# Kernel tuning notes

Hardware: AMD Instinct MI355X
Metric: run time of the kernel (lower is better)

The kernel has to match this reference:

```python
import jax, jax.numpy as jnp
import numpy as np

D = 64
NU = 30000
NI = 20000
LU = 50  # mailbox length at user nodes (item_max_length)
LI = 50  # mailbox length at item nodes (user_max_length)


def setup_inputs() -> dict:
    key = jax.random.key(0)
    ks = jax.random.split(key, 14)
    s = 0.05
    return {
        "user_feat": jax.random.normal(ks[0], (NU, D), jnp.float32),
        "item_feat": jax.random.normal(ks[1], (NI, D), jnp.float32),
        "W_u": jax.random.normal(ks[2], (D, D), jnp.float32) * s,
        "W_i": jax.random.normal(ks[3], (D, D), jnp.float32) * s,
        "Wg_u": jax.random.normal(ks[4], (2 * D, D), jnp.float32) * s,
        "Wg_i": jax.random.normal(ks[5], (2 * D, D), jnp.float32) * s,
        "i_te": jax.random.normal(ks[6], (LI, D), jnp.float32) * s,
        "i_te_k": jax.random.normal(ks[7], (LI, D), jnp.float32) * s,
        "u_te": jax.random.normal(ks[8], (LU, D), jnp.float32) * s,
        "u_te_k": jax.random.normal(ks[9], (LU, D), jnp.float32) * s,
        "item_nbr": jax.random.randint(ks[10], (NI, LI), 0, NU, jnp.int32),
        "item_time": jax.random.randint(ks[11], (NI, LI), 0, 1000000, jnp.int32),
        "user_nbr": jax.random.randint(ks[12], (NU, LU), 0, NI, jnp.int32),
        "user_time": jax.random.randint(ks[13], (NU, LU), 0, 1000000, jnp.int32),
    }


def _orgat_att(src_mb, dst_h, time, te, te_k):
    """One DGSR reduce: long-term time-encoded attention + short-term last-attention.
    src_mb: [N, L, d] gathered source features; dst_h: [N, d]; time: [N, L] int.
    Returns concat([h_long, h_short]) @ Wg applied by caller.
    """
    L = time.shape[1]
    d = src_mb.shape[-1]
    scale = jnp.sqrt(jnp.asarray(d, src_mb.dtype))
    # rank of each edge's time within the neighborhood; re_order: 0 = most recent
    rank = jnp.argsort(jnp.argsort(time, axis=1), axis=1)
    re_o = L - rank - 1                                       # [N, L]
    e = jnp.sum((te[re_o] + src_mb) * dst_h[:, None, :], axis=2) / scale
    alpha = jax.nn.softmax(e, axis=1)                         # [N, L]
    h_long = jnp.sum(alpha[..., None] * (src_mb + te_k[re_o]), axis=1)
    # short-term: attention keyed on the most-recent neighbor
    last = jnp.argmax(time, axis=1)
    last_em = jnp.take_along_axis(src_mb, last[:, None, None], axis=1)  # [N,1,d]
    e1 = jnp.sum(last_em * src_mb, axis=2) / scale
    a1 = jax.nn.softmax(e1, axis=1)
    h_short = jnp.sum(a1[..., None] * src_mb, axis=1)
    return jnp.concatenate([h_long, h_short], axis=-1)        # [N, 2d]


def reference(user_feat, item_feat, W_u, W_i, Wg_u, Wg_i, i_te, i_te_k,
              u_te, u_te_k, item_nbr, item_time, user_nbr, user_time):
    uh = user_feat @ W_u   # user_weight (feat_drop=0)
    ih = item_feat @ W_i   # item_weight
    # 'by' edges: users -> items (item reduce uses user mailboxes + i_time_encoding)
    u_mb = uh[item_nbr]                                        # [NI, LI, d]
    item_new = _orgat_att(u_mb, ih, item_time, i_te, i_te_k) @ Wg_i
    # 'pby' edges: items -> users (user reduce uses item mailboxes + u_time_encoding)
    i_mb = ih[user_nbr]                                        # [NU, LU, d]
    user_new = _orgat_att(i_mb, uh, user_time, u_te, u_te_k) @ Wg_u
    # residual update functions
    user_out = jax.nn.elu(user_new + user_feat)
    item_out = jax.nn.elu(item_new + item_feat)
    return user_out, item_out
```

## Files before the change

### kernel.cpp

```cpp
#include <hip/hip_runtime.h>
#include <stdint.h>

#define D   64
#define L   50
#define NUM_U 30000
#define NUM_I 20000


typedef __attribute__((ext_vector_type(8))) short short8x;
typedef __attribute__((ext_vector_type(4))) float f32x4;

__device__ __forceinline__ float lof(unsigned int u) {
    union { unsigned int i; float f; } v; v.i = u << 16; return v.f;
}
__device__ __forceinline__ float hif(unsigned int u) {
    union { unsigned int i; float f; } v; v.i = u & 0xffff0000u; return v.f;
}
__device__ __forceinline__ unsigned int f2bfbits(float f) {
    union { float f; unsigned int i; } v; v.f = f;
    return (v.i + 0x7fffu + ((v.i >> 16) & 1u)) >> 16;
}
__device__ __forceinline__ unsigned int packbf(float a, float b) {
    return f2bfbits(a) | (f2bfbits(b) << 16);
}
__device__ __forceinline__ float rl(float v, int l) {
    return __int_as_float(__builtin_amdgcn_readlane(__float_as_int(v), l));
}
__device__ __forceinline__ int rli(int v, int l) {
    return __builtin_amdgcn_readlane(v, l);
}

__global__ void pack_aux(const float* __restrict__ Wg_i, const float* __restrict__ Wg_u,
                         const float* __restrict__ te_i, const float* __restrict__ te_u,
                         const float* __restrict__ tk_i, const float* __restrict__ tk_u,
                         unsigned short* __restrict__ WgPi, unsigned short* __restrict__ WgPu,
                         unsigned short* __restrict__ tePi, unsigned short* __restrict__ tePu,
                         unsigned short* __restrict__ tkPi, unsigned short* __restrict__ tkPu)
{
    int gid = blockIdx.x * 256 + threadIdx.x, gs = gridDim.x * 256;
    for (int idx = gid; idx < 8192; idx += gs) {
        int n = idx >> 7, k = idx & 127;
        WgPi[idx] = (unsigned short)f2bfbits(Wg_i[k * 64 + n]);
        WgPu[idx] = (unsigned short)f2bfbits(Wg_u[k * 64 + n]);
    }
    for (int idx = gid; idx < 4096; idx += gs) {
        int r = idx >> 6, k = idx & 63;
        tePi[idx] = (r < L) ? (unsigned short)f2bfbits(te_i[r * 64 + k]) : 0;
        tePu[idx] = (r < L) ? (unsigned short)f2bfbits(te_u[r * 64 + k]) : 0;
        int d = idx >> 6, rr = idx & 63;
        tkPi[idx] = (rr < L) ? (unsigned short)f2bfbits(tk_i[rr * 64 + d]) : 0;
        tkPu[idx] = (rr < L) ? (unsigned short)f2bfbits(tk_u[rr * 64 + d]) : 0;
    }
}

__global__ __launch_bounds__(256) void gemm_h(
    const float* __restrict__ user_feat,
    const float* __restrict__ item_feat,
    const float* __restrict__ W_u,
    const float* __restrict__ W_i,
    unsigned int* __restrict__ H)
{
    const int tid = threadIdx.x, lane = tid & 63, wid = tid >> 6;
    int r0 = blockIdx.x * 16 + wid * 4;
    const float* src; const float* W;
    if (r0 < NUM_U) { src = user_feat + (size_t)r0 * D;            W = W_u; }
    else            { src = item_feat + (size_t)(r0 - NUM_U) * D;  W = W_i; }

    float f0 = src[0 * D + lane], f1 = src[1 * D + lane];
    float f2 = src[2 * D + lane], f3 = src[3 * D + lane];
    float a0 = 0.f, a1 = 0.f, a2 = 0.f, a3 = 0.f;
#pragma unroll
    for (int k = 0; k < 64; k++) {
        float wk = W[k * 64 + lane];
        a0 += rl(f0, k) * wk; a1 += rl(f1, k) * wk;
        a2 += rl(f2, k) * wk; a3 += rl(f3, k) * wk;
    }
    int li = (lane & 31) << 1;
    float p0 = __shfl(a0, li), q0 = __shfl(a0, li | 1);
    float p1 = __shfl(a1, li), q1 = __shfl(a1, li | 1);
    float p2 = __shfl(a2, li), q2 = __shfl(a2, li | 1);
    float p3 = __shfl(a3, li), q3 = __shfl(a3, li | 1);
    if (lane < 32) {
        H[(size_t)(r0 + 0) * 32 + lane] = packbf(p0, q0);
        H[(size_t)(r0 + 1) * 32 + lane] = packbf(p1, q1);
        H[(size_t)(r0 + 2) * 32 + lane] = packbf(p2, q2);
        H[(size_t)(r0 + 3) * 32 + lane] = packbf(p3, q3);
    }
}

__global__ __launch_bounds__(256, 4) void attn_ws(
    const unsigned int* __restrict__ H,
    int src_base, int dst_base,
    const float* __restrict__ dst_feat,
    const unsigned short* __restrict__ WgP,
    const unsigned short* __restrict__ teP,
    const unsigned short* __restrict__ tekP,
    const int* __restrict__ nbr,
    const int* __restrict__ timev,
    float* __restrict__ out)
{
    __shared__ unsigned int   mbs[4][56 * 33];
    __shared__ float          esc[4][192];
    __shared__ unsigned short ala[4][192];
    __shared__ unsigned short dhlm[4][128];
    __shared__ unsigned short cat16[4][136];

    const int tid = threadIdx.x, lane = tid & 63, wid = tid >> 6;
    const int n = blockIdx.x * 4 + wid;
    const int q4 = lane >> 4, c16 = lane & 15;

    unsigned int* mbw = mbs[wid];
    unsigned short* mbw_sh = (unsigned short*)mbw;

    for (int p = lane; p < 198; p += 64) mbw[1650 + p] = 0;

    int t   = (lane < L) ? timev[(size_t)n * L + lane] : 0;
    int nbv = (lane < L) ? nbr[(size_t)n * L + lane]  : 0;
    unsigned int key  = (lane < L) ? ((((unsigned)t) << 6) | (unsigned)lane) : 0u;
    unsigned int key2 = (lane < L) ? ((((unsigned)t) << 6) | (unsigned)(63 - lane)) : 0u;

    int rank = 0;
#pragma unroll
    for (int j = 0; j < L; j++) {
        unsigned int kj = (unsigned int)rli((int)key, j);
        rank += (kj < key) ? 1 : 0;
    }
    int re_o = (lane < L) ? (L - 1 - rank) : lane;

    unsigned int m2 = key2;
#pragma unroll
    for (int s = 32; s; s >>= 1) { unsigned int o2 = __shfl_xor(m2, s); m2 = (o2 > m2) ? o2 : m2; }
    const int last = 63 - (int)(m2 & 63u);

    unsigned int ud = H[(size_t)(dst_base + n) * 32 + (lane >> 1)];
    float dh = (lane & 1) ? hif(ud) : lof(ud);
    dhlm[wid][lane] = (unsigned short)f2bfbits(dh);

    {
        const unsigned int* Hs = H + (size_t)src_base * 32;
        int half = lane >> 5, col = lane & 31;
#pragma unroll
        for (int l = 0; l < L; l += 2) {
            int ra = rli(nbv, l), rb = rli(nbv, l + 1);
            int r = half ? rb : ra;
            mbw[(l + half) * 33 + col] = Hs[(size_t)r * 32 + col];
        }
    }

    unsigned int ulm = mbw[last * 33 + (lane >> 1)];
    float lm = (lane & 1) ? hif(ulm) : lof(ulm);
    dhlm[wid][64 + lane] = (unsigned short)f2bfbits(lm);

    f32x4 zero4 = {0.f, 0.f, 0.f, 0.f};
    f32x4 acc_e[4], acc_t[4];
#pragma unroll
    for (int nt = 0; nt < 4; nt++) { acc_e[nt] = zero4; acc_t[nt] = zero4; }
    {
        const unsigned short* dl = dhlm[wid];
#pragma unroll
        for (int kt = 0; kt < 2; kt++) {
            short8x afr = *(const short8x*)(dl + (c16 & 1) * 64 + kt * 32 + q4 * 8);
#pragma unroll
            for (int nt = 0; nt < 4; nt++) {
                int row = c16 + 16 * nt;
                union { short8x v; unsigned int u[4]; } bu;
                int base = row * 33 + kt * 16 + q4 * 4;
                bu.u[0] = mbw[base + 0]; bu.u[1] = mbw[base + 1];
                bu.u[2] = mbw[base + 2]; bu.u[3] = mbw[base + 3];
                acc_e[nt] = __builtin_amdgcn_mfma_f32_16x16x32_bf16(afr, bu.v, acc_e[nt], 0, 0, 0);
                short8x bt = *(const short8x*)(teP + row * 64 + kt * 32 + q4 * 8);
                acc_t[nt] = __builtin_amdgcn_mfma_f32_16x16x32_bf16(afr, bt, acc_t[nt], 0, 0, 0);
            }
        }
    }
    if (q4 == 0) {
#pragma unroll
        for (int nt = 0; nt < 4; nt++) {
            esc[wid][c16 + 16 * nt]       = acc_e[nt][0];
            esc[wid][64 + c16 + 16 * nt]  = acc_e[nt][1];
            esc[wid][128 + c16 + 16 * nt] = acc_t[nt][0];
        }
    }
    float e  = esc[wid][lane];
    float e1 = esc[wid][64 + lane];
    float th = esc[wid][128 + re_o];

    e = (e + th) * 0.125f;
    e1 *= 0.125f;
    if (lane >= L) { e = -3e38f; e1 = -3e38f; }

    float mx = e;
#pragma unroll
    for (int s = 32; s; s >>= 1) { float o2 = __shfl_xor(mx, s); mx = (o2 > mx) ? o2 : mx; }
    float ex = __expf(e - mx);
    float sm = ex;
#pragma unroll
    for (int s = 32; s; s >>= 1) sm += __shfl_xor(sm, s);
    float alpha = ex / sm;

    float mx1 = e1;
#pragma unroll
    for (int s = 32; s; s >>= 1) { float o2 = __shfl_xor(mx1, s); mx1 = (o2 > mx1) ? o2 : mx1; }
    float ex1 = __expf(e1 - mx1);
    float sm1 = ex1;
#pragma unroll
    for (int s = 32; s; s >>= 1) sm1 += __shfl_xor(sm1, s);
    float aw = ex1 / sm1;

    ala[wid][lane]        = (unsigned short)f2bfbits(alpha);
    ala[wid][64 + lane]   = (unsigned short)f2bfbits(aw);
    ala[wid][128 + re_o]  = (unsigned short)f2bfbits(alpha);

    f32x4 acc_s[4], acc_k[4];
#pragma unroll
    for (int nt = 0; nt < 4; nt++) { acc_s[nt] = zero4; acc_k[nt] = zero4; }
    {
        const unsigned short* alp = ala[wid];
#pragma unroll
        for (int kt = 0; kt < 2; kt++) {
            short8x aS = *(const short8x*)(alp + (c16 & 1) * 64 + kt * 32 + q4 * 8);
            short8x aB = *(const short8x*)(alp + 128 + kt * 32 + q4 * 8);
#pragma unroll
            for (int nt = 0; nt < 4; nt++) {
                int dcol = c16 + 16 * nt;
                short8x bM;
                if (kt == 0) {
                    int b0 = (q4 * 8) * 66 + dcol;
#pragma unroll
                    for (int i = 0; i < 8; i++) bM[i] = (short)mbw_sh[b0 + i * 66];
                } else {
#pragma unroll
                    for (int i = 0; i < 8; i++) {
                        int k = 32 + q4 * 8 + i;
                        int kk = (k < L) ? k : L;
                        bM[i] = (short)mbw_sh[kk * 66 + dcol];
                    }
                }
                acc_s[nt] = __builtin_amdgcn_mfma_f32_16x16x32_bf16(aS, bM, acc_s[nt], 0, 0, 0);
                short8x bK = *(const short8x*)(tekP + dcol * 64 + kt * 32 + q4 * 8);
                acc_k[nt] = __builtin_amdgcn_mfma_f32_16x16x32_bf16(aB, bK, acc_k[nt], 0, 0, 0);
            }
        }
    }
    if (q4 == 0) {
#pragma unroll
        for (int nt = 0; nt < 4; nt++) {
            cat16[wid][c16 + 16 * nt]      = (unsigned short)f2bfbits(acc_s[nt][0] + acc_k[nt][0]);
            cat16[wid][64 + c16 + 16 * nt] = (unsigned short)f2bfbits(acc_s[nt][1]);
        }
    }
    __syncthreads();

    short8x bfr[4];
#pragma unroll
    for (int tK = 0; tK < 4; tK++)
        bfr[tK] = *(const short8x*)(WgP + (wid * 16 + c16) * 128 + tK * 32 + q4 * 8);

    f32x4 acc = zero4;
#pragma unroll
    for (int tK = 0; tK < 4; tK++) {
        short8x a = *(const short8x*)(&cat16[lane & 3][tK * 32 + q4 * 8]);
        acc = __builtin_amdgcn_mfma_f32_16x16x32_bf16(a, bfr[tK], acc, 0, 0, 0);
    }
    float r01 = (q4 & 1) ? acc[1] : acc[0];
    float r23 = (q4 & 1) ? acc[3] : acc[2];
    float pv  = (q4 & 2) ? r23 : r01;

    int node = blockIdx.x * 4 + q4;
    float fres = dst_feat[(size_t)node * D + wid * 16 + c16];
    float oo = pv + fres;
    oo = (oo > 0.f) ? oo : (__expf(oo) - 1.f);
    out[(size_t)node * D + wid * 16 + c16] = oo;
}

__global__ __launch_bounds__(256) void attn_mono(
    const float* __restrict__ src_feat, const float* __restrict__ dst_feat,
    const float* __restrict__ W_src, const float* __restrict__ W_dst,
    const float* __restrict__ Wg, const float* __restrict__ te,
    const float* __restrict__ tek, const int* __restrict__ nbr,
    const int* __restrict__ timev, float* __restrict__ out)
{
    __shared__ unsigned int ws32[64 * 33];
    __shared__ unsigned int te32[L * 33];
    __shared__ unsigned int mbs[4][L * 33];
    const int tid = threadIdx.x, lane = tid & 63, wid = tid >> 6;
    const int n = blockIdx.x * 4 + wid;
    {
        const float2* Wf2 = (const float2*)W_src;
        const float2* Te2 = (const float2*)te;
        for (int idx = tid; idx < 2048; idx += 256) {
            float2 w = Wf2[idx];
            ws32[(idx >> 5) * 33 + (idx & 31)] = packbf(w.x, w.y);
            if (idx < 1600) {
                float2 t2 = Te2[idx];
                te32[(idx >> 5) * 33 + (idx & 31)] = packbf(t2.x, t2.y);
            }
        }
    }
    __syncthreads();
    int t  = (lane < L) ? timev[(size_t)n * L + lane] : 0;
    int nb = (lane < L) ? nbr[(size_t)n * L + lane]  : 0;
    unsigned int key  = (lane < L) ? ((((unsigned)t) << 6) | (unsigned)lane) : 0u;
    unsigned int key2 = (lane < L) ? ((((unsigned)t) << 6) | (unsigned)(63 - lane)) : 0u;
    int rank = 0;
#pragma unroll
    for (int j = 0; j < L; j++) {
        unsigned int kj = (unsigned int)rli((int)key, j);
        rank += (kj < key) ? 1 : 0;
    }
    int re_o = (lane < L) ? (L - 1 - rank) : 0;
    unsigned int m2 = key2;
#pragma unroll
    for (int s = 32; s; s >>= 1) { unsigned int o2 = __shfl_xor(m2, s); m2 = (o2 > m2) ? o2 : m2; }
    const int last = 63 - (int)(m2 & 63u);
    const int rr = (lane < L) ? lane : (L - 1);
    float f = dst_feat[(size_t)n * D + lane];
    float dh;
    {
        float b0 = 0.f, b1 = 0.f, b2 = 0.f, b3 = 0.f;
#pragma unroll
        for (int k = 0; k < 64; k += 4) {
            b0 += rl(f, k + 0) * W_dst[(k + 0) * 64 + lane];
            b1 += rl(f, k + 1) * W_dst[(k + 1) * 64 + lane];
            b2 += rl(f, k + 2) * W_dst[(k + 2) * 64 + lane];
            b3 += rl(f, k + 3) * W_dst[(k + 3) * 64 + lane];
        }
        dh = (b0 + b1) + (b2 + b3);
    }
    float v1;
    {
        float b0 = 0.f, b1 = 0.f, b2 = 0.f, b3 = 0.f;
#pragma unroll
        for (int j = 0; j < 32; j += 2) {
            unsigned int u0 = ws32[lane * 33 + j];
            unsigned int u1 = ws32[lane * 33 + j + 1];
            b0 += lof(u0) * rl(dh, 2 * j + 0);
            b1 += hif(u0) * rl(dh, 2 * j + 1);
            b2 += lof(u1) * rl(dh, 2 * j + 2);
            b3 += hif(u1) * rl(dh, 2 * j + 3);
        }
        v1 = (b0 + b1) + (b2 + b3);
    }
    unsigned int* mbw = mbs[wid];
    {
        const float2* src2 = (const float2*)src_feat;
        int half = lane >> 5, col = lane & 31;
#pragma unroll
        for (int l = 0; l < L; l += 2) {
            int ra = rli(nb, l), rb = rli(nb, l + 1);
            int r = half ? rb : ra;
            float2 v = src2[(size_t)r * 32 + col];
            mbw[(l + half) * 33 + col] = packbf(v.x, v.y);
        }
    }
    __syncthreads();
    unsigned int ul = mbw[last * 33 + (lane >> 1)];
    float rlast = (lane & 1) ? hif(ul) : lof(ul);
    float g;
    {
        float b0 = 0.f, b1 = 0.f, b2 = 0.f, b3 = 0.f;
#pragma unroll
        for (int k = 0; k < 64; k += 4) {
            b0 += rl(rlast, k + 0) * W_src[(k + 0) * 64 + lane];
            b1 += rl(rlast, k + 1) * W_src[(k + 1) * 64 + lane];
            b2 += rl(rlast, k + 2) * W_src[(k + 2) * 64 + lane];
            b3 += rl(rlast, k + 3) * W_src[(k + 3) * 64 + lane];
        }
        g = (b0 + b1) + (b2 + b3);
    }
    float v2;
    {
        float b0 = 0.f, b1 = 0.f, b2 = 0.f, b3 = 0.f;
#pragma unroll
        for (int j = 0; j < 32; j += 2) {
            unsigned int u0 = ws32[lane * 33 + j];
            unsigned int u1 = ws32[lane * 33 + j + 1];
            b0 += lof(u0) * rl(g, 2 * j + 0);
            b1 += hif(u0) * rl(g, 2 * j + 1);
            b2 += lof(u1) * rl(g, 2 * j + 2);
            b3 += hif(u1) * rl(g, 2 * j + 3);
        }
        v2 = (b0 + b1) + (b2 + b3);
    }
    float teh;
    {
        float b0 = 0.f, b1 = 0.f, b2 = 0.f, b3 = 0.f;
#pragma unroll
        for (int j = 0; j < 32; j += 2) {
            unsigned int u0 = te32[rr * 33 + j];
            unsigned int u1 = te32[rr * 33 + j + 1];
            b0 += lof(u0) * rl(dh, 2 * j + 0);
            b1 += hif(u0) * rl(dh, 2 * j + 1);
            b2 += lof(u1) * rl(dh, 2 * j + 2);
            b3 += hif(u1) * rl(dh, 2 * j + 3);
        }
        teh = (b0 + b1) + (b2 + b3);
    }
    float e, e1;
    {
        float ea = 0.f, eb = 0.f, qa = 0.f, qb = 0.f;
#pragma unroll
        for (int j = 0; j < 32; j += 2) {
            unsigned int u0 = mbw[rr * 33 + j];
            unsigned int u1 = mbw[rr * 33 + j + 1];
            float m0 = lof(u0), m1 = hif(u0), m2f = lof(u1), m3 = hif(u1);
            ea += m0 * rl(v1, 2 * j + 0) + m1 * rl(v1, 2 * j + 1);
            eb += m2f * rl(v1, 2 * j + 2) + m3 * rl(v1, 2 * j + 3);
            qa += m0 * rl(v2, 2 * j + 0) + m1 * rl(v2, 2 * j + 1);
            qb += m2f * rl(v2, 2 * j + 2) + m3 * rl(v2, 2 * j + 3);
        }
        e = ea + eb; e1 = qa + qb;
    }
    e = (e + __shfl(teh, re_o)) * 0.125f;
    e1 *= 0.125f;
    if (lane >= L) { e = -3e38f; e1 = -3e38f; }
    float mx = e;
#pragma unroll
    for (int s = 32; s; s >>= 1) { float o2 = __shfl_xor(mx, s); mx = (o2 > mx) ? o2 : mx; }
    float ex = __expf(e - mx);
    float sm = ex;
#pragma unroll
    for (int s = 32; s; s >>= 1) sm += __shfl_xor(sm, s);
    float alpha = ex / sm;
    float mx1 = e1;
#pragma unroll
    for (int s = 32; s; s >>= 1) { float o2 = __shfl_xor(mx1, s); mx1 = (o2 > mx1) ? o2 : mx1; }
    float ex1 = __expf(e1 - mx1);
    float sm1 = ex1;
#pragma unroll
    for (int s = 32; s; s >>= 1) sm1 += __shfl_xor(sm1, s);
    float aw = ex1 / sm1;
    float sl, ss, tacc;
    {
        float sA = 0.f, sB = 0.f, hA = 0.f, hB = 0.f, tA = 0.f, tB = 0.f;
        int hcol = lane >> 1, odd = lane & 1;
#pragma unroll
        for (int l = 0; l < L; l += 2) {
            float saA = rl(alpha, l),     s1A = rl(aw, l);
            float saB = rl(alpha, l + 1), s1B = rl(aw, l + 1);
            int   roA = rli(re_o, l),     roB = rli(re_o, l + 1);
            unsigned int uA = mbw[(l + 0) * 33 + hcol];
            unsigned int uB = mbw[(l + 1) * 33 + hcol];
            float mA = odd ? hif(uA) : lof(uA);
            float mB = odd ? hif(uB) : lof(uB);
            sA += saA * mA; hA += s1A * mA; tA += saA * tek[roA * 64 + lane];
            sB += saB * mB; hB += s1B * mB; tB += saB * tek[roB * 64 + lane];
        }
        sl = sA + sB; ss = hA + hB; tacc = tA + tB;
    }
    float hl, hs;
    {
        float lA = 0.f, lB = 0.f, sA = 0.f, sB = 0.f;
#pragma unroll
        for (int k = 0; k < 64; k += 2) {
            float w0 = W_src[(k + 0) * 64 + lane];
            float w1 = W_src[(k + 1) * 64 + lane];
            lA += rl(sl, k + 0) * w0; sA += rl(ss, k + 0) * w0;
            lB += rl(sl, k + 1) * w1; sB += rl(ss, k + 1) * w1;
        }
        hl = tacc + lA + lB; hs = sA + sB;
    }
    float o;
    {
        float o0 = 0.f, o1 = 0.f, o2 = 0.f, o3 = 0.f;
#pragma unroll
        for (int k = 0; k < 64; k += 2) {
            o0 += rl(hl, k + 0) * Wg[(k + 0) * 64 + lane];
            o1 += rl(hl, k + 1) * Wg[(k + 1) * 64 + lane];
            o2 += rl(hs, k + 0) * Wg[(k + 64) * 64 + lane];
            o3 += rl(hs, k + 1) * Wg[(k + 65) * 64 + lane];
        }
        o = f + (o0 + o1) + (o2 + o3);
    }
    o = (o > 0.f) ? o : (__expf(o) - 1.f);
    out[(size_t)n * D + lane] = o;
}

extern "C" void kernel_launch(void* const* d_in, const int* in_sizes, int n_in,
                              void* d_out, int out_size, void* d_ws, size_t ws_size,
                              hipStream_t stream) {
    const float* user_feat = (const float*)d_in[0];
    const float* item_feat = (const float*)d_in[1];
    const float* W_u  = (const float*)d_in[2];
    const float* W_i  = (const float*)d_in[3];
    const float* Wg_u = (const float*)d_in[4];
    const float* Wg_i = (const float*)d_in[5];
    const float* i_te   = (const float*)d_in[6];
    const float* i_te_k = (const float*)d_in[7];
    const float* u_te   = (const float*)d_in[8];
    const float* u_te_k = (const float*)d_in[9];
    const int* item_nbr  = (const int*)d_in[10];
    const int* item_time = (const int*)d_in[11];
    const int* user_nbr  = (const int*)d_in[12];
    const int* user_time = (const int*)d_in[13];
    (void)in_sizes; (void)n_in; (void)out_size;

    float* outp = (float*)d_out;
    const size_t H_BYTES = (size_t)(NUM_U + NUM_I) * 32 * 4;
    const size_t NEED = H_BYTES + 2 * 16384 + 4 * 8192;

    if (ws_size >= NEED) {
        unsigned int* Hp = (unsigned int*)d_ws;
        unsigned char* aux = (unsigned char*)d_ws + H_BYTES;
        unsigned short* WgPi = (unsigned short*)(aux);
        unsigned short* WgPu = (unsigned short*)(aux + 16384);
        unsigned short* tePi = (unsigned short*)(aux + 32768);
        unsigned short* tePu = (unsigned short*)(aux + 40960);
        unsigned short* tkPi = (unsigned short*)(aux + 49152);
        unsigned short* tkPu = (unsigned short*)(aux + 57344);

        pack_aux<<<16, 256, 0, stream>>>(Wg_i, Wg_u, i_te, u_te, i_te_k, u_te_k,
                                         WgPi, WgPu, tePi, tePu, tkPi, tkPu);
        gemm_h<<<(NUM_U + NUM_I) / 16, 256, 0, stream>>>(
            user_feat, item_feat, W_u, W_i, Hp);
        attn_ws<<<NUM_I / 4, 256, 0, stream>>>(
            Hp, 0, NUM_U, item_feat, WgPi, tePi, tkPi,
            item_nbr, item_time, outp + (size_t)NUM_U * D);
        attn_ws<<<NUM_U / 4, 256, 0, stream>>>(
            Hp, NUM_U, 0, user_feat, WgPu, tePu, tkPu,
            user_nbr, user_time, outp);
    } else {
        attn_mono<<<NUM_I / 4, 256, 0, stream>>>(
            user_feat, item_feat, W_u, W_i, Wg_i, i_te, i_te_k,
            item_nbr, item_time, outp + (size_t)NUM_U * D);
        attn_mono<<<NUM_U / 4, 256, 0, stream>>>(
            item_feat, user_feat, W_i, W_u, Wg_u, u_te, u_te_k,
            user_nbr, user_time, outp);
    }
}
```

Before: 245.0 us.

## Merge prep kernels and fuse item/user attention launches with compact LDS layout

```diff
diff --git a/kernel.cpp b/kernel.cpp
--- a/kernel.cpp
+++ b/kernel.cpp
@@ -5,6 +5,7 @@
 #define L   50
 #define NUM_U 30000
 #define NUM_I 20000
+#define PW  1976
 
 
 typedef __attribute__((ext_vector_type(8))) short short8x;
@@ -30,89 +31,99 @@
     return __builtin_amdgcn_readlane(v, l);
 }
 
-__global__ void pack_aux(const float* __restrict__ Wg_i, const float* __restrict__ Wg_u,
-                         const float* __restrict__ te_i, const float* __restrict__ te_u,
-                         const float* __restrict__ tk_i, const float* __restrict__ tk_u,
-                         unsigned short* __restrict__ WgPi, unsigned short* __restrict__ WgPu,
-                         unsigned short* __restrict__ tePi, unsigned short* __restrict__ tePu,
-                         unsigned short* __restrict__ tkPi, unsigned short* __restrict__ tkPu)
+__global__ __launch_bounds__(256) void prep(
+    const float* __restrict__ user_feat, const float* __restrict__ item_feat,
+    const float* __restrict__ W_u, const float* __restrict__ W_i,
+    const float* __restrict__ Wg_i, const float* __restrict__ Wg_u,
+    const float* __restrict__ te_i, const float* __restrict__ te_u,
+    const float* __restrict__ tk_i, const float* __restrict__ tk_u,
+    unsigned int* __restrict__ H,
+    unsigned short* __restrict__ WgPi, unsigned short* __restrict__ WgPu,
+    unsigned short* __restrict__ tePi, unsigned short* __restrict__ tePu,
+    unsigned short* __restrict__ tkPi, unsigned short* __restrict__ tkPu)
 {
-    int gid = blockIdx.x * 256 + threadIdx.x, gs = gridDim.x * 256;
-    for (int idx = gid; idx < 8192; idx += gs) {
-        int n = idx >> 7, k = idx & 127;
-        WgPi[idx] = (unsigned short)f2bfbits(Wg_i[k * 64 + n]);
-        WgPu[idx] = (unsigned short)f2bfbits(Wg_u[k * 64 + n]);
-    }
-    for (int idx = gid; idx < 4096; idx += gs) {
-        int r = idx >> 6, k = idx & 63;
-        tePi[idx] = (r < L) ? (unsigned short)f2bfbits(te_i[r * 64 + k]) : 0;
-        tePu[idx] = (r < L) ? (unsigned short)f2bfbits(te_u[r * 64 + k]) : 0;
-        int d = idx >> 6, rr = idx & 63;
-        tkPi[idx] = (rr < L) ? (unsigned short)f2bfbits(tk_i[rr * 64 + d]) : 0;
-        tkPu[idx] = (rr < L) ? (unsigned short)f2bfbits(tk_u[rr * 64 + d]) : 0;
-    }
-}
-
-__global__ __launch_bounds__(256) void gemm_h(
-    const float* __restrict__ user_feat,
-    const float* __restrict__ item_feat,
-    const float* __restrict__ W_u,
-    const float* __restrict__ W_i,
-    unsigned int* __restrict__ H)
-{
-    const int tid = threadIdx.x, lane = tid & 63, wid = tid >> 6;
-    int r0 = blockIdx.x * 16 + wid * 4;
-    const float* src; const float* W;
-    if (r0 < NUM_U) { src = user_feat + (size_t)r0 * D;            W = W_u; }
-    else            { src = item_feat + (size_t)(r0 - NUM_U) * D;  W = W_i; }
-
-    float f0 = src[0 * D + lane], f1 = src[1 * D + lane];
-    float f2 = src[2 * D + lane], f3 = src[3 * D + lane];
-    float a0 = 0.f, a1 = 0.f, a2 = 0.f, a3 = 0.f;
-#pragma unroll
-    for (int k = 0; k < 64; k++) {
-        float wk = W[k * 64 + lane];
-        a0 += rl(f0, k) * wk; a1 += rl(f1, k) * wk;
-        a2 += rl(f2, k) * wk; a3 += rl(f3, k) * wk;
-    }
-    int li = (lane & 31) << 1;
-    float p0 = __shfl(a0, li), q0 = __shfl(a0, li | 1);
-    float p1 = __shfl(a1, li), q1 = __shfl(a1, li | 1);
-    float p2 = __shfl(a2, li), q2 = __shfl(a2, li | 1);
-    float p3 = __shfl(a3, li), q3 = __shfl(a3, li | 1);
-    if (lane < 32) {
-        H[(size_t)(r0 + 0) * 32 + lane] = packbf(p0, q0);
-        H[(size_t)(r0 + 1) * 32 + lane] = packbf(p1, q1);
-        H[(size_t)(r0 + 2) * 32 + lane] = packbf(p2, q2);
-        H[(size_t)(r0 + 3) * 32 + lane] = packbf(p3, q3);
-    }
-}
-
-__global__ __launch_bounds__(256, 4) void attn_ws(
+    const int tid = threadIdx.x;
+    if (blockIdx.x < 3125) {
+        const int lane = tid & 63, wid = tid >> 6;
+        int r0 = blockIdx.x * 16 + wid * 4;
+        const float* src; const float* W;
+        if (r0 < NUM_U) { src = user_feat + (size_t)r0 * D;            W = W_u; }
+        else            { src = item_feat + (size_t)(r0 - NUM_U) * D;  W = W_i; }
+        float f0 = src[0 * D + lane], f1 = src[1 * D + lane];
+        float f2 = src[2 * D + lane], f3 = src[3 * D + lane];
+        float a0 = 0.f, a1 = 0.f, a2 = 0.f, a3 = 0.f;
+#pragma unroll
+        for (int k = 0; k < 64; k++) {
+            float wk = W[k * 64 + lane];
+            a0 += rl(f0, k) * wk; a1 += rl(f1, k) * wk;
+            a2 += rl(f2, k) * wk; a3 += rl(f3, k) * wk;
+        }
+        int li = (lane & 31) << 1;
+        float p0 = __shfl(a0, li), q0 = __shfl(a0, li | 1);
+        float p1 = __shfl(a1, li), q1 = __shfl(a1, li | 1);
+        float p2 = __shfl(a2, li), q2 = __shfl(a2, li | 1);
+        float p3 = __shfl(a3, li), q3 = __shfl(a3, li | 1);
+        if (lane < 32) {
+            H[(size_t)(r0 + 0) * 32 + lane] = packbf(p0, q0);
+            H[(size_t)(r0 + 1) * 32 + lane] = packbf(p1, q1);
+            H[(size_t)(r0 + 2) * 32 + lane] = packbf(p2, q2);
+            H[(size_t)(r0 + 3) * 32 + lane] = packbf(p3, q3);
+        }
+    } else {
+        int gid = (blockIdx.x - 3125) * 256 + tid;
+        for (int idx = gid; idx < 8192; idx += 4096) {
+            int n = idx >> 7, k = idx & 127;
+            WgPi[idx] = (unsigned short)f2bfbits(Wg_i[k * 64 + n]);
+            WgPu[idx] = (unsigned short)f2bfbits(Wg_u[k * 64 + n]);
+        }
+        {
+            int idx = gid;
+            int r = idx >> 6, k = idx & 63;
+            tePi[idx] = (r < L) ? (unsigned short)f2bfbits(te_i[r * 64 + k]) : 0;
+            tePu[idx] = (r < L) ? (unsigned short)f2bfbits(te_u[r * 64 + k]) : 0;
+            int d = idx >> 6, rr = idx & 63;
+            tkPi[idx] = (rr < L) ? (unsigned short)f2bfbits(tk_i[rr * 64 + d]) : 0;
+            tkPu[idx] = (rr < L) ? (unsigned short)f2bfbits(tk_u[rr * 64 + d]) : 0;
+        }
+    }
+}
+
+__global__ __launch_bounds__(256, 5) void attn_fused(
     const unsigned int* __restrict__ H,
-    int src_base, int dst_base,
-    const float* __restrict__ dst_feat,
-    const unsigned short* __restrict__ WgP,
-    const unsigned short* __restrict__ teP,
-    const unsigned short* __restrict__ tekP,
-    const int* __restrict__ nbr,
-    const int* __restrict__ timev,
+    const float* __restrict__ user_feat, const float* __restrict__ item_feat,
+    const unsigned short* __restrict__ WgPi, const unsigned short* __restrict__ WgPu,
+    const unsigned short* __restrict__ tePi, const unsigned short* __restrict__ tePu,
+    const unsigned short* __restrict__ tkPi, const unsigned short* __restrict__ tkPu,
+    const int* __restrict__ item_nbr, const int* __restrict__ item_time,
+    const int* __restrict__ user_nbr, const int* __restrict__ user_time,
     float* __restrict__ out)
 {
-    __shared__ unsigned int   mbs[4][56 * 33];
-    __shared__ float          esc[4][192];
-    __shared__ unsigned short ala[4][192];
-    __shared__ unsigned short dhlm[4][128];
-    __shared__ unsigned short cat16[4][136];
+    __shared__ unsigned int lds[4 * PW];
 
     const int tid = threadIdx.x, lane = tid & 63, wid = tid >> 6;
-    const int n = blockIdx.x * 4 + wid;
+    const bool iside = blockIdx.x < (NUM_I / 4);
+    const int bb = iside ? blockIdx.x : blockIdx.x - NUM_I / 4;
+    const int n = bb * 4 + wid;
+    const int src_base = iside ? 0 : NUM_U;
+    const int dst_base = iside ? NUM_U : 0;
+    const float* dst_feat = iside ? item_feat : user_feat;
+    const unsigned short* WgP  = iside ? WgPi : WgPu;
+    const unsigned short* teP  = iside ? tePi : tePu;
+    const unsigned short* tekP = iside ? tkPi : tkPu;
+    const int* nbr   = iside ? item_nbr  : user_nbr;
+    const int* timev = iside ? item_time : user_time;
+    float* outp = out + (iside ? (size_t)NUM_U * D : 0);
+
     const int q4 = lane >> 4, c16 = lane & 15;
 
-    unsigned int* mbw = mbs[wid];
+    unsigned int*   wld    = lds + wid * PW;
+    unsigned int*   mbw    = wld;
     unsigned short* mbw_sh = (unsigned short*)mbw;
-
-    for (int p = lane; p < 198; p += 64) mbw[1650 + p] = 0;
+    float*          escf   = (float*)(wld + 1684);
+    unsigned short* cat    = (unsigned short*)(wld + 1684);
+    unsigned short* dla    = (unsigned short*)(wld + 1876);
+
+    if (lane < 33) mbw[1650 + lane] = 0;
 
     int t   = (lane < L) ? timev[(size_t)n * L + lane] : 0;
     int nbv = (lane < L) ? nbr[(size_t)n * L + lane]  : 0;
@@ -134,7 +145,7 @@
 
     unsigned int ud = H[(size_t)(dst_base + n) * 32 + (lane >> 1)];
     float dh = (lane & 1) ? hif(ud) : lof(ud);
-    dhlm[wid][lane] = (unsigned short)f2bfbits(dh);
+    dla[lane] = (unsigned short)f2bfbits(dh);
 
     {
         const unsigned int* Hs = H + (size_t)src_base * 32;
@@ -149,41 +160,39 @@
 
     unsigned int ulm = mbw[last * 33 + (lane >> 1)];
     float lm = (lane & 1) ? hif(ulm) : lof(ulm);
-    dhlm[wid][64 + lane] = (unsigned short)f2bfbits(lm);
+    dla[64 + lane] = (unsigned short)f2bfbits(lm);
 
     f32x4 zero4 = {0.f, 0.f, 0.f, 0.f};
     f32x4 acc_e[4], acc_t[4];
 #pragma unroll
     for (int nt = 0; nt < 4; nt++) { acc_e[nt] = zero4; acc_t[nt] = zero4; }
-    {
-        const unsigned short* dl = dhlm[wid];
-#pragma unroll
-        for (int kt = 0; kt < 2; kt++) {
-            short8x afr = *(const short8x*)(dl + (c16 & 1) * 64 + kt * 32 + q4 * 8);
-#pragma unroll
-            for (int nt = 0; nt < 4; nt++) {
-                int row = c16 + 16 * nt;
-                union { short8x v; unsigned int u[4]; } bu;
-                int base = row * 33 + kt * 16 + q4 * 4;
-                bu.u[0] = mbw[base + 0]; bu.u[1] = mbw[base + 1];
-                bu.u[2] = mbw[base + 2]; bu.u[3] = mbw[base + 3];
-                acc_e[nt] = __builtin_amdgcn_mfma_f32_16x16x32_bf16(afr, bu.v, acc_e[nt], 0, 0, 0);
-                short8x bt = *(const short8x*)(teP + row * 64 + kt * 32 + q4 * 8);
-                acc_t[nt] = __builtin_amdgcn_mfma_f32_16x16x32_bf16(afr, bt, acc_t[nt], 0, 0, 0);
-            }
+#pragma unroll
+    for (int kt = 0; kt < 2; kt++) {
+        short8x afr = *(const short8x*)(dla + (c16 & 1) * 64 + kt * 32 + q4 * 8);
+#pragma unroll
+        for (int nt = 0; nt < 4; nt++) {
+            int row = c16 + 16 * nt;
+            int rowc = (row > 50) ? 50 : row;
+            union { short8x v; unsigned int u[4]; } bu;
+            int base = rowc * 33 + kt * 16 + q4 * 4;
+            bu.u[0] = mbw[base + 0]; bu.u[1] = mbw[base + 1];
+            bu.u[2] = mbw[base + 2]; bu.u[3] = mbw[base + 3];
+            acc_e[nt] = __builtin_amdgcn_mfma_f32_16x16x32_bf16(afr, bu.v, acc_e[nt], 0, 0, 0);
+            short8x bt = *(const short8x*)(teP + row * 64 + kt * 32 + q4 * 8);
+            acc_t[nt] = __builtin_amdgcn_mfma_f32_16x16x32_bf16(afr, bt, acc_t[nt], 0, 0, 0);
         }
     }
     if (q4 == 0) {
 #pragma unroll
         for (int nt = 0; nt < 4; nt++) {
-            esc[wid][c16 + 16 * nt]       = acc_e[nt][0];
-            esc[wid][64 + c16 + 16 * nt]  = acc_e[nt][1];
-            esc[wid][128 + c16 + 16 * nt] = acc_t[nt][0];
-        }
-    }
-    float e  = esc[wid][lane];
-    float e1 = esc[wid][64 + lane];
-    float th = esc[wid][128 + re_o];
+            escf[c16 + 16 * nt]       = acc_e[nt][0];
+            escf[64 + c16 + 16 * nt]  = acc_e[nt][1];
+            escf[128 + c16 + 16 * nt] = acc_t[nt][0];
+        }
+    }
+    float e  = escf[lane];
+    float e1 = escf[64 + lane];
+    float th = escf[128 + re_o];
 
     e = (e + th) * 0.125f;
     e1 *= 0.125f;
@@ -207,46 +216,43 @@
     for (int s = 32; s; s >>= 1) sm1 += __shfl_xor(sm1, s);
     float aw = ex1 / sm1;
 
-    ala[wid][lane]        = (unsigned short)f2bfbits(alpha);
-    ala[wid][64 + lane]   = (unsigned short)f2bfbits(aw);
-    ala[wid][128 + re_o]  = (unsigned short)f2bfbits(alpha);
+    dla[lane]       = (unsigned short)f2bfbits(alpha);
+    dla[64 + lane]  = (unsigned short)f2bfbits(aw);
+    dla[128 + re_o] = (unsigned short)f2bfbits(alpha);
 
     f32x4 acc_s[4], acc_k[4];
 #pragma unroll
     for (int nt = 0; nt < 4; nt++) { acc_s[nt] = zero4; acc_k[nt] = zero4; }
-    {
-        const unsigned short* alp = ala[wid];
-#pragma unroll
-        for (int kt = 0; kt < 2; kt++) {
-            short8x aS = *(const short8x*)(alp + (c16 & 1) * 64 + kt * 32 + q4 * 8);
-            short8x aB = *(const short8x*)(alp + 128 + kt * 32 + q4 * 8);
-#pragma unroll
-            for (int nt = 0; nt < 4; nt++) {
-                int dcol = c16 + 16 * nt;
-                short8x bM;
-                if (kt == 0) {
-                    int b0 = (q4 * 8) * 66 + dcol;
-#pragma unroll
-                    for (int i = 0; i < 8; i++) bM[i] = (short)mbw_sh[b0 + i * 66];
-                } else {
-#pragma unroll
-                    for (int i = 0; i < 8; i++) {
-                        int k = 32 + q4 * 8 + i;
-                        int kk = (k < L) ? k : L;
-                        bM[i] = (short)mbw_sh[kk * 66 + dcol];
-                    }
+#pragma unroll
+    for (int kt = 0; kt < 2; kt++) {
+        short8x aS = *(const short8x*)(dla + (c16 & 1) * 64 + kt * 32 + q4 * 8);
+        short8x aB = *(const short8x*)(dla + 128 + kt * 32 + q4 * 8);
+#pragma unroll
+        for (int nt = 0; nt < 4; nt++) {
+            int dcol = c16 + 16 * nt;
+            short8x bM;
+            if (kt == 0) {
+                int b0 = (q4 * 8) * 66 + dcol;
+#pragma unroll
+                for (int i = 0; i < 8; i++) bM[i] = (short)mbw_sh[b0 + i * 66];
+            } else {
+#pragma unroll
+                for (int i = 0; i < 8; i++) {
+                    int k = 32 + q4 * 8 + i;
+                    int kk = (k < L) ? k : 50;
+                    bM[i] = (short)mbw_sh[kk * 66 + dcol];
                 }
-                acc_s[nt] = __builtin_amdgcn_mfma_f32_16x16x32_bf16(aS, bM, acc_s[nt], 0, 0, 0);
-                short8x bK = *(const short8x*)(tekP + dcol * 64 + kt * 32 + q4 * 8);
-                acc_k[nt] = __builtin_amdgcn_mfma_f32_16x16x32_bf16(aB, bK, acc_k[nt], 0, 0, 0);
             }
+            acc_s[nt] = __builtin_amdgcn_mfma_f32_16x16x32_bf16(aS, bM, acc_s[nt], 0, 0, 0);
+            short8x bK = *(const short8x*)(tekP + dcol * 64 + kt * 32 + q4 * 8);
+            acc_k[nt] = __builtin_amdgcn_mfma_f32_16x16x32_bf16(aB, bK, acc_k[nt], 0, 0, 0);
         }
     }
     if (q4 == 0) {
 #pragma unroll
         for (int nt = 0; nt < 4; nt++) {
-            cat16[wid][c16 + 16 * nt]      = (unsigned short)f2bfbits(acc_s[nt][0] + acc_k[nt][0]);
-            cat16[wid][64 + c16 + 16 * nt] = (unsigned short)f2bfbits(acc_s[nt][1]);
+            cat[c16 + 16 * nt]      = (unsigned short)f2bfbits(acc_s[nt][0] + acc_k[nt][0]);
+            cat[64 + c16 + 16 * nt] = (unsigned short)f2bfbits(acc_s[nt][1]);
         }
     }
     __syncthreads();
@@ -256,21 +262,22 @@
     for (int tK = 0; tK < 4; tK++)
         bfr[tK] = *(const short8x*)(WgP + (wid * 16 + c16) * 128 + tK * 32 + q4 * 8);
 
+    const unsigned short* catw = (const unsigned short*)(lds + (lane & 3) * PW + 1684);
     f32x4 acc = zero4;
 #pragma unroll
     for (int tK = 0; tK < 4; tK++) {
-        short8x a = *(const short8x*)(&cat16[lane & 3][tK * 32 + q4 * 8]);
+        short8x a = *(const short8x*)(catw + tK * 32 + q4 * 8);
         acc = __builtin_amdgcn_mfma_f32_16x16x32_bf16(a, bfr[tK], acc, 0, 0, 0);
     }
     float r01 = (q4 & 1) ? acc[1] : acc[0];
     float r23 = (q4 & 1) ? acc[3] : acc[2];
     float pv  = (q4 & 2) ? r23 : r01;
 
-    int node = blockIdx.x * 4 + q4;
+    int node = bb * 4 + q4;
     float fres = dst_feat[(size_t)node * D + wid * 16 + c16];
     float oo = pv + fres;
     oo = (oo > 0.f) ? oo : (__expf(oo) - 1.f);
-    out[(size_t)node * D + wid * 16 + c16] = oo;
+    outp[(size_t)node * D + wid * 16 + c16] = oo;
 }
 
 __global__ __launch_bounds__(256) void attn_mono(
@@ -509,16 +516,12 @@
         unsigned short* tkPi = (unsigned short*)(aux + 49152);
         unsigned short* tkPu = (unsigned short*)(aux + 57344);
 
-        pack_aux<<<16, 256, 0, stream>>>(Wg_i, Wg_u, i_te, u_te, i_te_k, u_te_k,
-                                         WgPi, WgPu, tePi, tePu, tkPi, tkPu);
-        gemm_h<<<(NUM_U + NUM_I) / 16, 256, 0, stream>>>(
-            user_feat, item_feat, W_u, W_i, Hp);
-        attn_ws<<<NUM_I / 4, 256, 0, stream>>>(
-            Hp, 0, NUM_U, item_feat, WgPi, tePi, tkPi,
-            item_nbr, item_time, outp + (size_t)NUM_U * D);
-        attn_ws<<<NUM_U / 4, 256, 0, stream>>>(
-            Hp, NUM_U, 0, user_feat, WgPu, tePu, tkPu,
-            user_nbr, user_time, outp);
+        prep<<<3141, 256, 0, stream>>>(user_feat, item_feat, W_u, W_i,
+                                       Wg_i, Wg_u, i_te, u_te, i_te_k, u_te_k,
+                                       Hp, WgPi, WgPu, tePi, tePu, tkPi, tkPu);
+        attn_fused<<<(NUM_I + NUM_U) / 4, 256, 0, stream>>>(
+            Hp, user_feat, item_feat, WgPi, WgPu, tePi, tePu, tkPi, tkPu,
+            item_nbr, item_time, user_nbr, user_time, outp);
     } else {
         attn_mono<<<NUM_I / 4, 256, 0, stream>>>(
             user_feat, item_feat, W_u, W_i, Wg_i, i_te, i_te_k,
```

Measured after the change: 241.5 us. No clear change (-1.4%).
